# Kernel tuning notes

Hardware: AMD Instinct MI355X
Metric: run time of the kernel (lower is better)

Reference implementation:

```python
import jax, jax.numpy as jnp
import numpy as np

EPS = 1e-6


def rms_norm(x, w):
    xf = x.astype(jnp.float32)
    var = jnp.mean(xf * xf, axis=-1, keepdims=True)
    return (xf * jax.lax.rsqrt(var + EPS)).astype(x.dtype) * w


def rope_interleaved(x, cos, sin):
    # x: [B, S, D]; rotate interleaved pairs (even=real, odd=imag)
    B, S, D = x.shape
    xp = x.reshape(B, S, D // 2, 2)
    rot = jnp.stack([-xp[..., 1], xp[..., 0]], axis=-1).reshape(B, S, D)
    return (x.astype(jnp.float32) * cos + rot.astype(jnp.float32) * sin).astype(x.dtype)


def setup_inputs() -> dict:
    key = jax.random.key(0)
    ks = jax.random.split(key, 8)
    B, S, D = 1, 2048, 2048
    H, Dh = 32, 64
    std = 1.0 / np.sqrt(D)

    hidden_states = jax.random.normal(ks[0], (B, S, D), jnp.float32)

    # interleaved RoPE tables tiled across heads -> [1, S, D]
    pos = np.arange(S, dtype=np.float64)
    inv_freq = 1.0 / (10000.0 ** (np.arange(0, Dh, 2, dtype=np.float64) / Dh))
    ang = pos[:, None] * inv_freq[None, :]          # [S, Dh/2]
    ang = np.repeat(ang, 2, axis=-1)                 # [S, Dh] interleaved
    ang = np.tile(ang, (1, H))                       # [S, D]
    cos = jnp.asarray(np.cos(ang)[None], jnp.float32)
    sin = jnp.asarray(np.sin(ang)[None], jnp.float32)

    Wq = jax.random.normal(ks[1], (D, D), jnp.float32) * std
    Wk = jax.random.normal(ks[2], (D, D), jnp.float32) * std
    Wv = jax.random.normal(ks[3], (D, D), jnp.float32) * std
    Wo = jax.random.normal(ks[4], (D, D), jnp.float32) * std
    bq = jax.random.normal(ks[5], (D,), jnp.float32) * 0.02
    bk = jax.random.normal(ks[6], (D,), jnp.float32) * 0.02
    bv = jax.random.normal(ks[7], (D,), jnp.float32) * 0.02
    bo = jnp.zeros((D,), jnp.float32)
    q_norm_w = jnp.ones((D,), jnp.float32)
    k_norm_w = jnp.ones((D,), jnp.float32)
    return {
        "hidden_states": hidden_states, "cos": cos, "sin": sin,
        "Wq": Wq, "bq": bq, "Wk": Wk, "bk": bk, "Wv": Wv, "bv": bv,
        "q_norm_w": q_norm_w, "k_norm_w": k_norm_w, "Wo": Wo, "bo": bo,
    }


def reference(hidden_states, cos, sin, Wq, bq, Wk, bk, Wv, bv, q_norm_w, k_norm_w, Wo, bo):
    B, S, D = hidden_states.shape
    H, Dh = 32, 64
    # QKV projections (self-attention: encoder_hidden_states = hidden_states)
    q = hidden_states @ Wq + bq
    k = hidden_states @ Wk + bk
    v = hidden_states @ Wv + bv
    # RMSNorm across heads (over full inner_dim)
    q = rms_norm(q, q_norm_w)
    k = rms_norm(k, k_norm_w)
    # interleaved rotary embedding (key uses query rope when key rope is None)
    q = rope_interleaved(q, cos, sin)
    k = rope_interleaved(k, cos, sin)
    # split heads: [B, H, S, Dh]
    q = q.reshape(B, S, H, Dh).transpose(0, 2, 1, 3)
    k = k.reshape(B, S, H, Dh).transpose(0, 2, 1, 3)
    v = v.reshape(B, S, H, Dh).transpose(0, 2, 1, 3)
    # scaled dot-product attention (no mask, not causal)
    scale = 1.0 / jnp.sqrt(jnp.asarray(Dh, q.dtype))
    scores = jnp.einsum("bhqd,bhkd->bhqk", q, k) * scale
    attn = jax.nn.softmax(scores, axis=-1)
    out = jnp.einsum("bhqk,bhkd->bhqd", attn, v)
    out = out.transpose(0, 2, 1, 3).reshape(B, S, H * Dh)
    return out @ Wo + bo
```

## Files before the change

kernel.cpp:

```cpp
#include <hip/hip_runtime.h>
#include <hip/hip_bf16.h>

typedef __bf16 bf16_t;
typedef __bf16 bf16x8 __attribute__((ext_vector_type(8)));
typedef __bf16 bf16x4 __attribute__((ext_vector_type(4)));
typedef float floatx4 __attribute__((ext_vector_type(4)));
typedef float floatx16 __attribute__((ext_vector_type(16)));

#define S_LEN 2048
#define D_DIM 2048
#define NHEADS 32
#define DH 64

__device__ __forceinline__ void gll16(const bf16_t* g, bf16_t* l) {
    __builtin_amdgcn_global_load_lds(
        (const __attribute__((address_space(1))) unsigned int*)g,
        (__attribute__((address_space(3))) unsigned int*)l, 16, 0, 0);
}

#define BAR()    asm volatile("s_barrier" ::: "memory")
#define WAIT(N)  asm volatile("s_waitcnt vmcnt(" #N ")" ::: "memory")
#define DSWAIT() asm volatile("s_waitcnt lgkmcnt(0)" ::: "memory")

__global__ __launch_bounds__(256) void k_prep(
    const float* __restrict__ hs, bf16_t* __restrict__ Xb,
    const float* __restrict__ W0, const float* __restrict__ W1,
    const float* __restrict__ W2, const float* __restrict__ W3,
    bf16_t* __restrict__ T0, bf16_t* __restrict__ T1,
    bf16_t* __restrict__ T2, bf16_t* __restrict__ T3)
{
    const int t = threadIdx.x;
    if (blockIdx.z == 4) {
        const int bid = blockIdx.y * 32 + blockIdx.x;
        const int i = (bid * 256 + t) * 16;
        const float4 a0 = *(const float4*)(hs + i);
        const float4 a1 = *(const float4*)(hs + i + 4);
        const float4 a2 = *(const float4*)(hs + i + 8);
        const float4 a3 = *(const float4*)(hs + i + 12);
        bf16x8 o0, o1;
        o0[0]=(bf16_t)a0.x; o0[1]=(bf16_t)a0.y; o0[2]=(bf16_t)a0.z; o0[3]=(bf16_t)a0.w;
        o0[4]=(bf16_t)a1.x; o0[5]=(bf16_t)a1.y; o0[6]=(bf16_t)a1.z; o0[7]=(bf16_t)a1.w;
        o1[0]=(bf16_t)a2.x; o1[1]=(bf16_t)a2.y; o1[2]=(bf16_t)a2.z; o1[3]=(bf16_t)a2.w;
        o1[4]=(bf16_t)a3.x; o1[5]=(bf16_t)a3.y; o1[6]=(bf16_t)a3.z; o1[7]=(bf16_t)a3.w;
        *(bf16x8*)(Xb + i) = o0;
        *(bf16x8*)(Xb + i + 8) = o1;
        return;
    }
    const float* W; bf16_t* T;
    switch (blockIdx.z) {
        case 0: W = W0; T = T0; break;
        case 1: W = W1; T = T1; break;
        case 2: W = W2; T = T2; break;
        default: W = W3; T = T3; break;
    }
    __shared__ float tile_t[64][68];
    const int n0 = blockIdx.x * 64, k0 = blockIdx.y * 64;
    #pragma unroll
    for (int i = 0; i < 16; ++i) {
        const int r = i * 4 + (t >> 6);
        const int c = t & 63;
        tile_t[c][r] = W[(size_t)(k0 + r) * D_DIM + n0 + c];
    }
    __syncthreads();
    #pragma unroll
    for (int j = 0; j < 4; ++j) {
        const int n  = j * 16 + (t >> 4);
        const int k4 = (t & 15) * 4;
        const float4 v = *(const float4*)&tile_t[n][k4];
        bf16x4 pk;
        pk[0] = (bf16_t)v.x; pk[1] = (bf16_t)v.y; pk[2] = (bf16_t)v.z; pk[3] = (bf16_t)v.w;
        *(bf16x4*)(T + (size_t)(n0 + n) * D_DIM + k0 + k4) = pk;
    }
}

#define BM 128
#define BN 128
#define BK 32

__global__ __launch_bounds__(256) void k_gemm_qkv(
    const bf16_t* __restrict__ A,
    const bf16_t* __restrict__ Bt0, const bf16_t* __restrict__ Bt1, const bf16_t* __restrict__ Bt2,
    const float* __restrict__ bias0, const float* __restrict__ bias1, const float* __restrict__ bias2,
    bf16_t* __restrict__ Qout, bf16_t* __restrict__ Kout, bf16_t* __restrict__ VtOut,
    int M, int N, int K)
{
    const bf16_t* Bt; const float* bias;
    if (blockIdx.z == 0)      { Bt = Bt0; bias = bias0; }
    else if (blockIdx.z == 1) { Bt = Bt1; bias = bias1; }
    else                      { Bt = Bt2; bias = bias2; }

    __shared__ bf16_t As[3][BM][BK];
    __shared__ bf16_t Bs[3][BN][BK];

    const int t    = threadIdx.x;
    const int lane = t & 63;
    const int wave = t >> 6;
    const int wm = (wave >> 1) * 64;
    const int wn = (wave & 1) * 64;
    const int bm = blockIdx.y * BM;
    const int bn = blockIdx.x * BN;
    const int lm = lane & 15;
    const int lq = lane >> 4;

    const int srow0 = wave * 32 + (lane >> 2);
    const int srow1 = srow0 + 16;
    const int cp    = lane & 3;
    const int gc0 = cp ^ ((srow0 >> 1) & 3);
    const int gc1 = cp ^ ((srow1 >> 1) & 3);

    const bf16_t* Ag0 = A  + (size_t)(bm + srow0) * K + gc0 * 8;
    const bf16_t* Ag1 = A  + (size_t)(bm + srow1) * K + gc1 * 8;
    const bf16_t* Bg0 = Bt + (size_t)(bn + srow0) * K + gc0 * 8;
    const bf16_t* Bg1 = Bt + (size_t)(bn + srow1) * K + gc1 * 8;

    floatx4 acc[4][4];
    #pragma unroll
    for (int i = 0; i < 4; ++i)
        #pragma unroll
        for (int j = 0; j < 4; ++j)
            #pragma unroll
            for (int r = 0; r < 4; ++r) acc[i][j][r] = 0.f;

    const int NIT = K / BK;
    auto stage = [&](int buf, int k0) {
        gll16(Ag0 + k0, &As[buf][wave * 32][0]);
        gll16(Ag1 + k0, &As[buf][wave * 32 + 16][0]);
        gll16(Bg0 + k0, &Bs[buf][wave * 32][0]);
        gll16(Bg1 + k0, &Bs[buf][wave * 32 + 16][0]);
    };
    stage(0, 0);
    stage(1, BK);

    for (int i = 0; i < NIT; ++i) {
        BAR();
        if (i + 2 < NIT) {
            stage((i + 2) % 3, (i + 2) * BK);
            WAIT(8);
        } else if (i + 1 < NIT) {
            WAIT(4);
        } else {
            WAIT(0);
        }
        BAR();

        const int buf = i % 3;
        bf16x8 af[4], bfr[4];
        #pragma unroll
        for (int ii = 0; ii < 4; ++ii) {
            const int row = wm + ii * 16 + lm;
            af[ii] = *(const bf16x8*)&As[buf][row][(lq ^ ((row >> 1) & 3)) * 8];
        }
        #pragma unroll
        for (int j = 0; j < 4; ++j) {
            const int row = wn + j * 16 + lm;
            bfr[j] = *(const bf16x8*)&Bs[buf][row][(lq ^ ((row >> 1) & 3)) * 8];
        }
        #pragma unroll
        for (int ii = 0; ii < 4; ++ii)
            #pragma unroll
            for (int j = 0; j < 4; ++j)
                acc[ii][j] = __builtin_amdgcn_mfma_f32_16x16x32_bf16(af[ii], bfr[j], acc[ii][j], 0, 0, 0);
    }

    if (blockIdx.z == 2) {
        #pragma unroll
        for (int i = 0; i < 4; ++i) {
            const int row0 = bm + wm + i * 16 + lq * 4;
            #pragma unroll
            for (int j = 0; j < 4; ++j) {
                const int col = bn + wn + j * 16 + lm;
                const float bb = bias[col];
                bf16x4 pk;
                #pragma unroll
                for (int r = 0; r < 4; ++r) pk[r] = (bf16_t)(acc[i][j][r] + bb);
                *(bf16x4*)(VtOut + (size_t)col * M + row0) = pk;
            }
        }
    } else {
        bf16_t* C = (blockIdx.z == 0) ? Qout : Kout;
        #pragma unroll
        for (int i = 0; i < 4; ++i) {
            const int row0 = bm + wm + i * 16 + lq * 4;
            #pragma unroll
            for (int j = 0; j < 4; ++j) {
                const int col = bn + wn + j * 16 + lm;
                const float bb = bias[col];
                #pragma unroll
                for (int r = 0; r < 4; ++r)
                    C[(size_t)(row0 + r) * N + col] = (bf16_t)(acc[i][j][r] + bb);
            }
        }
    }
}

__global__ __launch_bounds__(256) void k_gemm_splitk(
    const bf16_t* __restrict__ A, const bf16_t* __restrict__ Bt,
    float* __restrict__ P0, float* __restrict__ P1, float* __restrict__ P2,
    int M, int N, int K)
{
    __shared__ bf16_t As[3][BM][BK];
    __shared__ bf16_t Bs[3][BN][BK];

    const int t    = threadIdx.x;
    const int lane = t & 63;
    const int wave = t >> 6;
    const int wm = (wave >> 1) * 64;
    const int wn = (wave & 1) * 64;
    const int bm = blockIdx.y * BM;
    const int bn = blockIdx.x * BN;
    const int lm = lane & 15;
    const int lq = lane >> 4;
    const int z  = blockIdx.z;

    const int nit_all = K / BK;
    const int it0 = (z * nit_all) / 3;
    const int it1 = ((z + 1) * nit_all) / 3;
    const int NIT = it1 - it0;
    const int kbase = it0 * BK;

    const int srow0 = wave * 32 + (lane >> 2);
    const int srow1 = srow0 + 16;
    const int cp    = lane & 3;
    const int gc0 = cp ^ ((srow0 >> 1) & 3);
    const int gc1 = cp ^ ((srow1 >> 1) & 3);

    const bf16_t* Ag0 = A  + (size_t)(bm + srow0) * K + kbase + gc0 * 8;
    const bf16_t* Ag1 = A  + (size_t)(bm + srow1) * K + kbase + gc1 * 8;
    const bf16_t* Bg0 = Bt + (size_t)(bn + srow0) * K + kbase + gc0 * 8;
    const bf16_t* Bg1 = Bt + (size_t)(bn + srow1) * K + kbase + gc1 * 8;

    floatx4 acc[4][4];
    #pragma unroll
    for (int i = 0; i < 4; ++i)
        #pragma unroll
        for (int j = 0; j < 4; ++j)
            #pragma unroll
            for (int r = 0; r < 4; ++r) acc[i][j][r] = 0.f;

    auto stage = [&](int buf, int k0) {
        gll16(Ag0 + k0, &As[buf][wave * 32][0]);
        gll16(Ag1 + k0, &As[buf][wave * 32 + 16][0]);
        gll16(Bg0 + k0, &Bs[buf][wave * 32][0]);
        gll16(Bg1 + k0, &Bs[buf][wave * 32 + 16][0]);
    };
    stage(0, 0);
    if (1 < NIT) stage(1, BK);

    for (int i = 0; i < NIT; ++i) {
        BAR();
        if (i + 2 < NIT) {
            stage((i + 2) % 3, (i + 2) * BK);
            WAIT(8);
        } else if (i + 1 < NIT) {
            WAIT(4);
        } else {
            WAIT(0);
        }
        BAR();

        const int buf = i % 3;
        bf16x8 af[4], bfr[4];
        #pragma unroll
        for (int ii = 0; ii < 4; ++ii) {
            const int row = wm + ii * 16 + lm;
            af[ii] = *(const bf16x8*)&As[buf][row][(lq ^ ((row >> 1) & 3)) * 8];
        }
        #pragma unroll
        for (int j = 0; j < 4; ++j) {
            const int row = wn + j * 16 + lm;
            bfr[j] = *(const bf16x8*)&Bs[buf][row][(lq ^ ((row >> 1) & 3)) * 8];
        }
        #pragma unroll
        for (int ii = 0; ii < 4; ++ii)
            #pragma unroll
            for (int j = 0; j < 4; ++j)
                acc[ii][j] = __builtin_amdgcn_mfma_f32_16x16x32_bf16(af[ii], bfr[j], acc[ii][j], 0, 0, 0);
    }

    float* C = (z == 0) ? P0 : (z == 1) ? P1 : P2;
    #pragma unroll
    for (int i = 0; i < 4; ++i) {
        const int row0 = bm + wm + i * 16 + lq * 4;
        #pragma unroll
        for (int j = 0; j < 4; ++j) {
            const int col = bn + wn + j * 16 + lm;
            #pragma unroll
            for (int r = 0; r < 4; ++r)
                C[(size_t)(row0 + r) * N + col] = acc[i][j][r];
        }
    }
}

__global__ __launch_bounds__(256) void k_reduce_bias(
    const float* __restrict__ P0, const float* __restrict__ P1,
    const float* __restrict__ P2, const float* __restrict__ bias,
    float* __restrict__ out)
{
    const int i = (blockIdx.x * 256 + threadIdx.x) * 4;
    const float4 b  = *(const float4*)(bias + (i & (D_DIM - 1)));
    const float4 a0 = *(const float4*)(P0 + i);
    const float4 a1 = *(const float4*)(P1 + i);
    const float4 a2 = *(const float4*)(P2 + i);
    float4 o;
    o.x = b.x + a0.x + a1.x + a2.x;
    o.y = b.y + a0.y + a1.y + a2.y;
    o.z = b.z + a0.z + a1.z + a2.z;
    o.w = b.w + a0.w + a1.w + a2.w;
    *(float4*)(out + i) = o;
}

__global__ __launch_bounds__(256) void k_norm_rope(
    bf16_t* __restrict__ Q, bf16_t* __restrict__ Kb_,
    const float* __restrict__ qw, const float* __restrict__ kw,
    const float* __restrict__ cosb, const float* __restrict__ sinb)
{
    bf16_t* X = (blockIdx.z == 0) ? Q : Kb_;
    const float* w = (blockIdx.z == 0) ? qw : kw;
    const int row = blockIdx.x;
    const int t = threadIdx.x;
    const size_t base = (size_t)row * D_DIM + t * 8;

    const bf16x8 xv = *(const bf16x8*)(X + base);
    float x[8];
    #pragma unroll
    for (int i = 0; i < 8; ++i) x[i] = (float)xv[i];

    float ss = 0.f;
    #pragma unroll
    for (int i = 0; i < 8; ++i) ss += x[i] * x[i];
    #pragma unroll
    for (int off = 32; off; off >>= 1) ss += __shfl_xor(ss, off);
    __shared__ float red[4];
    if ((t & 63) == 0) red[t >> 6] = ss;
    __syncthreads();
    const float tot = red[0] + red[1] + red[2] + red[3];
    const float rms = rsqrtf(tot * (1.0f / D_DIM) + 1e-6f);

    float wv[8], c[8], sn[8];
    { float4 a = *(const float4*)(w + t * 8); float4 b = *(const float4*)(w + t * 8 + 4);
      wv[0]=a.x; wv[1]=a.y; wv[2]=a.z; wv[3]=a.w; wv[4]=b.x; wv[5]=b.y; wv[6]=b.z; wv[7]=b.w; }
    const size_t cbase = (size_t)row * D_DIM + ((t * 8) & 63);
    { float4 a = *(const float4*)(cosb + cbase); float4 b = *(const float4*)(cosb + cbase + 4);
      c[0]=a.x; c[1]=a.y; c[2]=a.z; c[3]=a.w; c[4]=b.x; c[5]=b.y; c[6]=b.z; c[7]=b.w; }
    { float4 a = *(const float4*)(sinb + cbase); float4 b = *(const float4*)(sinb + cbase + 4);
      sn[0]=a.x; sn[1]=a.y; sn[2]=a.z; sn[3]=a.w; sn[4]=b.x; sn[5]=b.y; sn[6]=b.z; sn[7]=b.w; }

    bf16x8 o;
    #pragma unroll
    for (int p = 0; p < 4; ++p) {
        const float e  = x[2*p]     * rms * wv[2*p];
        const float od = x[2*p + 1] * rms * wv[2*p + 1];
        o[2*p]     = (bf16_t)(e * c[2*p]     - od * sn[2*p]);
        o[2*p + 1] = (bf16_t)(od * c[2*p + 1] + e * sn[2*p + 1]);
    }
    *(bf16x8*)(X + base) = o;
}

#define LDPQ 72

__global__ __launch_bounds__(256) void k_flash(
    const bf16_t* __restrict__ Qb, const bf16_t* __restrict__ Kb,
    const bf16_t* __restrict__ Vt, bf16_t* __restrict__ Ob)
{
    const int bid = blockIdx.x;
    const int jj  = bid >> 3;
    const int h   = ((bid & 7) << 2) | (jj >> 4);
    const int qblk = jj & 15;
    const int hc = h * DH;
    const int t = threadIdx.x;
    const int wave = t >> 6, lane = t & 63;
    const int ln = lane & 31, hf = lane >> 5;
    const int qw = qblk * 128 + wave * 32;

    __shared__ bf16_t Ks[3][64][64];
    __shared__ bf16_t Vs[3][64][64];
    __shared__ bf16_t Ps[4][32][LDPQ];
    __shared__ float  Lw[4][32];

    bf16x8 bq[4];
    #pragma unroll
    for (int kt = 0; kt < 4; ++kt)
        bq[kt] = *(const bf16x8*)(Qb + (size_t)(qw + ln) * D_DIM + hc + kt * 16 + hf * 8);

    const int r0  = wave * 16 + (lane >> 3);
    const int r1  = r0 + 8;
    const int cp8 = lane & 7;
    const int gcA = cp8 ^ (r0 & 7);
    const int gcB = cp8 ^ (r1 & 7);
    const bf16_t* kg0 = Kb + (size_t)r0 * D_DIM + hc + gcA * 8;
    const bf16_t* kg1 = Kb + (size_t)r1 * D_DIM + hc + gcB * 8;
    const bf16_t* vg0 = Vt + (size_t)(hc + r0) * S_LEN + gcA * 8;
    const bf16_t* vg1 = Vt + (size_t)(hc + r1) * S_LEN + gcB * 8;

    auto stageKV = [&](int buf, int kc) {
        gll16(kg0 + (size_t)kc * D_DIM, &Ks[buf][wave * 16][0]);
        gll16(kg1 + (size_t)kc * D_DIM, &Ks[buf][wave * 16 + 8][0]);
        gll16(vg0 + kc, &Vs[buf][wave * 16][0]);
        gll16(vg1 + kc, &Vs[buf][wave * 16 + 8][0]);
    };

    floatx16 o0, o1;
    #pragma unroll
    for (int r = 0; r < 16; ++r) { o0[r] = 0.f; o1[r] = 0.f; }
    float lsum = 0.f;

    const int swz = ln & 7;
    const float c_exp = 0.125f * 1.44269504089f;
    const int NCH = S_LEN / 64;

    auto qk = [&](int buf, floatx16& s0, floatx16& s1) {
        #pragma unroll
        for (int r = 0; r < 16; ++r) { s0[r] = 0.f; s1[r] = 0.f; }
        #pragma unroll
        for (int kt = 0; kt < 4; ++kt) {
            const int ch = 2 * kt + hf;
            const bf16x8 a0 = *(const bf16x8*)&Ks[buf][ln]     [(ch ^ swz) * 8];
            const bf16x8 a1 = *(const bf16x8*)&Ks[buf][32 + ln][(ch ^ swz) * 8];
            s0 = __builtin_amdgcn_mfma_f32_32x32x16_bf16(a0, bq[kt], s0, 0, 0, 0);
            s1 = __builtin_amdgcn_mfma_f32_32x32x16_bf16(a1, bq[kt], s1, 0, 0, 0);
        }
    };
    auto expv = [&](const floatx16& s0, const floatx16& s1) {
        #pragma unroll
        for (int g = 0; g < 4; ++g) {
            bf16x4 p0, p1;
            #pragma unroll
            for (int r4 = 0; r4 < 4; ++r4) {
                const float e0 = __builtin_amdgcn_exp2f(s0[4 * g + r4] * c_exp);
                const float e1 = __builtin_amdgcn_exp2f(s1[4 * g + r4] * c_exp);
                p0[r4] = (bf16_t)e0; p1[r4] = (bf16_t)e1;
                lsum += e0 + e1;
            }
            *(bf16x4*)&Ps[wave][ln][8 * g + 4 * hf]      = p0;
            *(bf16x4*)&Ps[wave][ln][32 + 8 * g + 4 * hf] = p1;
        }
    };
    auto pv = [&](int buf) {
        #pragma unroll
        for (int kt = 0; kt < 4; ++kt) {
            const int ch = 2 * kt + hf;
            const bf16x8 ap  = *(const bf16x8*)&Ps[wave][ln][kt * 16 + hf * 8];
            const bf16x8 bv0 = *(const bf16x8*)&Vs[buf][ln]     [(ch ^ swz) * 8];
            const bf16x8 bv1 = *(const bf16x8*)&Vs[buf][32 + ln][(ch ^ swz) * 8];
            o0 = __builtin_amdgcn_mfma_f32_32x32x16_bf16(ap, bv0, o0, 0, 0, 0);
            o1 = __builtin_amdgcn_mfma_f32_32x32x16_bf16(ap, bv1, o1, 0, 0, 0);
        }
    };

    stageKV(0, 0);
    stageKV(1, 64);

    floatx16 stA0, stA1, stB0, stB1;

    auto pipe_step = [&](int c, floatx16& n0_, floatx16& n1_,
                         floatx16& p0_, floatx16& p1_) {
        BAR();
        if (c >= 1 && c + 1 < NCH) {
            stageKV((c + 1) % 3, (c + 1) * 64);
            WAIT(4);
        } else if (c == 0) {
            WAIT(4);
        } else {
            WAIT(0);
        }
        BAR();
        qk(c % 3, n0_, n1_);
        if (c > 0) {
            expv(p0_, p1_);
            DSWAIT();
            pv((c - 1) % 3);
        }
    };

    for (int c2 = 0; c2 < NCH; c2 += 2) {
        pipe_step(c2,     stA0, stA1, stB0, stB1);
        pipe_step(c2 + 1, stB0, stB1, stA0, stA1);
    }
    expv(stB0, stB1);
    DSWAIT();
    pv((NCH - 1) % 3);

    const float ltot = lsum + __shfl_xor(lsum, 32);
    if (hf == 0) Lw[wave][ln] = ltot;
    DSWAIT();
    float4 li[4];
    li[0] = *(const float4*)&Lw[wave][4 * hf];
    li[1] = *(const float4*)&Lw[wave][8 + 4 * hf];
    li[2] = *(const float4*)&Lw[wave][16 + 4 * hf];
    li[3] = *(const float4*)&Lw[wave][24 + 4 * hf];

    #pragma unroll
    for (int r = 0; r < 16; ++r) {
        const int row = (r & 3) + 8 * (r >> 2) + 4 * hf;
        const float lv = (r & 3) == 0 ? li[r >> 2].x : (r & 3) == 1 ? li[r >> 2].y
                       : (r & 3) == 2 ? li[r >> 2].z : li[r >> 2].w;
        const float inv = 1.0f / lv;
        Ob[(size_t)(qw + row) * D_DIM + hc + ln]      = (bf16_t)(o0[r] * inv);
        Ob[(size_t)(qw + row) * D_DIM + hc + 32 + ln] = (bf16_t)(o1[r] * inv);
    }
}

extern "C" void kernel_launch(void* const* d_in, const int* in_sizes, int n_in,
                              void* d_out, int out_size, void* d_ws, size_t ws_size,
                              hipStream_t stream) {
    const float* hs   = (const float*)d_in[0];
    const float* cosb = (const float*)d_in[1];
    const float* sinb = (const float*)d_in[2];
    const float* Wq   = (const float*)d_in[3];
    const float* bq   = (const float*)d_in[4];
    const float* Wk   = (const float*)d_in[5];
    const float* bk   = (const float*)d_in[6];
    const float* Wv   = (const float*)d_in[7];
    const float* bv   = (const float*)d_in[8];
    const float* qw   = (const float*)d_in[9];
    const float* kw   = (const float*)d_in[10];
    const float* Wo   = (const float*)d_in[11];
    const float* bo   = (const float*)d_in[12];
    float* out = (float*)d_out;

    char* ws = (char*)d_ws;
    bf16_t* Xb  = (bf16_t*)(ws);
    bf16_t* Wqt = (bf16_t*)(ws + ((size_t)8  << 20));
    bf16_t* Wkt = (bf16_t*)(ws + ((size_t)16 << 20));
    bf16_t* Wvt = (bf16_t*)(ws + ((size_t)24 << 20));
    bf16_t* Wot = (bf16_t*)(ws + ((size_t)32 << 20));
    bf16_t* Qb  = (bf16_t*)(ws + ((size_t)40 << 20));
    bf16_t* Kb  = (bf16_t*)(ws + ((size_t)48 << 20));
    bf16_t* Vt  = (bf16_t*)(ws + ((size_t)56 << 20));
    bf16_t* Ob  = (bf16_t*)(ws + ((size_t)64 << 20));
    float*  P0  = (float*) (ws);
    float*  P1  = (float*) (ws + ((size_t)16 << 20));
    float*  P2  = (float*) (ws + ((size_t)48 << 20));

    const int n = S_LEN * D_DIM;

    k_prep<<<dim3(32, 32, 5), 256, 0, stream>>>(hs, Xb, Wq, Wk, Wv, Wo, Wqt, Wkt, Wvt, Wot);

    k_gemm_qkv<<<dim3(D_DIM / BN, S_LEN / BM, 3), 256, 0, stream>>>(
        Xb, Wqt, Wkt, Wvt, bq, bk, bv, Qb, Kb, Vt, S_LEN, D_DIM, D_DIM);

    k_norm_rope<<<dim3(S_LEN, 1, 2), 256, 0, stream>>>(Qb, Kb, qw, kw, cosb, sinb);

    k_flash<<<512, 256, 0, stream>>>(Qb, Kb, Vt, Ob);

    k_gemm_splitk<<<dim3(D_DIM / BN, S_LEN / BM, 3), 256, 0, stream>>>(
        Ob, Wot, P0, P1, P2, S_LEN, D_DIM, D_DIM);
    k_reduce_bias<<<n / (256 * 4), 256, 0, stream>>>(P0, P1, P2, bo, out);
}
```

Baseline: 314.0 us.

## Restructure flash kernel to 2-wave blocks with double buffering and register-held V

The attention kernel now uses 128-thread blocks (two waves, 64 query rows) launched as 1024 blocks, switching from triple to double-buffered K/V staging. V fragments are loaded into registers for the current chunk and consumed one iteration later, so the V LDS buffer can be overwritten earlier. The P tile gets an XOR swizzle instead of padding, and the row-sum scratch reuses the P buffer. The aim is higher occupancy and less LDS per block, at the cost of more blocks each reloading K/V and extra register pressure from the held V fragments.

```diff
diff --git a/kernel.cpp b/kernel.cpp
--- a/kernel.cpp
+++ b/kernel.cpp
@@ -356,138 +356,151 @@
     *(bf16x8*)(X + base) = o;
 }
 
-#define LDPQ 72
-
-__global__ __launch_bounds__(256) void k_flash(
+__global__ __launch_bounds__(128, 2) void k_flash(
     const bf16_t* __restrict__ Qb, const bf16_t* __restrict__ Kb,
     const bf16_t* __restrict__ Vt, bf16_t* __restrict__ Ob)
 {
     const int bid = blockIdx.x;
-    const int jj  = bid >> 3;
-    const int h   = ((bid & 7) << 2) | (jj >> 4);
-    const int qblk = jj & 15;
+    const int h    = ((bid & 7) << 2) | (bid >> 8);
+    const int qblk = (bid >> 3) & 31;
     const int hc = h * DH;
     const int t = threadIdx.x;
     const int wave = t >> 6, lane = t & 63;
     const int ln = lane & 31, hf = lane >> 5;
-    const int qw = qblk * 128 + wave * 32;
-
-    __shared__ bf16_t Ks[3][64][64];
-    __shared__ bf16_t Vs[3][64][64];
-    __shared__ bf16_t Ps[4][32][LDPQ];
-    __shared__ float  Lw[4][32];
+    const int qw = qblk * 64 + wave * 32;
+
+    __shared__ bf16_t Ks[2][64][64];
+    __shared__ bf16_t Vs[2][64][64];
+    __shared__ bf16_t Ps[2][32][64];
 
     bf16x8 bq[4];
     #pragma unroll
     for (int kt = 0; kt < 4; ++kt)
         bq[kt] = *(const bf16x8*)(Qb + (size_t)(qw + ln) * D_DIM + hc + kt * 16 + hf * 8);
 
-    const int r0  = wave * 16 + (lane >> 3);
-    const int r1  = r0 + 8;
-    const int cp8 = lane & 7;
-    const int gcA = cp8 ^ (r0 & 7);
-    const int gcB = cp8 ^ (r1 & 7);
-    const bf16_t* kg0 = Kb + (size_t)r0 * D_DIM + hc + gcA * 8;
-    const bf16_t* kg1 = Kb + (size_t)r1 * D_DIM + hc + gcB * 8;
-    const bf16_t* vg0 = Vt + (size_t)(hc + r0) * S_LEN + gcA * 8;
-    const bf16_t* vg1 = Vt + (size_t)(hc + r1) * S_LEN + gcB * 8;
+    const int rr = wave * 32 + (lane >> 3);
+    const int gc = (lane & 7) ^ (lane >> 3);
+    const bf16_t* kg = Kb + (size_t)rr * D_DIM + hc + gc * 8;
+    const bf16_t* vg = Vt + (size_t)(hc + rr) * S_LEN + gc * 8;
 
     auto stageKV = [&](int buf, int kc) {
-        gll16(kg0 + (size_t)kc * D_DIM, &Ks[buf][wave * 16][0]);
-        gll16(kg1 + (size_t)kc * D_DIM, &Ks[buf][wave * 16 + 8][0]);
-        gll16(vg0 + kc, &Vs[buf][wave * 16][0]);
-        gll16(vg1 + kc, &Vs[buf][wave * 16 + 8][0]);
+        #pragma unroll
+        for (int i = 0; i < 4; ++i) {
+            gll16(kg + (size_t)(kc + 8 * i) * D_DIM, &Ks[buf][wave * 32 + 8 * i][0]);
+            gll16(vg + (size_t)(8 * i) * S_LEN + kc, &Vs[buf][wave * 32 + 8 * i][0]);
+        }
     };
 
-    floatx16 o0, o1;
+    floatx16 o0, o1, st;
     #pragma unroll
     for (int r = 0; r < 16; ++r) { o0[r] = 0.f; o1[r] = 0.f; }
     float lsum = 0.f;
+    bf16x8 vr[2][8];
 
     const int swz = ln & 7;
     const float c_exp = 0.125f * 1.44269504089f;
     const int NCH = S_LEN / 64;
 
-    auto qk = [&](int buf, floatx16& s0, floatx16& s1) {
-        #pragma unroll
-        for (int r = 0; r < 16; ++r) { s0[r] = 0.f; s1[r] = 0.f; }
+    auto qk = [&]() {
+        #pragma unroll
+        for (int r = 0; r < 16; ++r) st[r] = 0.f;
+    };
+    (void)qk;
+
+    floatx16 st1;
+
+    stageKV(0, 0);
+
+    for (int c = 0; c < NCH; ++c) {
+        const int cur = c & 1;
+        BAR();
+        if (c + 1 < NCH) {
+            stageKV(cur ^ 1, (c + 1) * 64);
+            WAIT(8);
+        } else {
+            WAIT(0);
+        }
+        BAR();
+
+        if (c > 0) {
+            #pragma unroll
+            for (int g = 0; g < 4; ++g) {
+                bf16x4 p0, p1;
+                #pragma unroll
+                for (int r4 = 0; r4 < 4; ++r4) {
+                    const float e0 = __builtin_amdgcn_exp2f(st[4 * g + r4] * c_exp);
+                    const float e1 = __builtin_amdgcn_exp2f(st1[4 * g + r4] * c_exp);
+                    p0[r4] = (bf16_t)e0; p1[r4] = (bf16_t)e1;
+                    lsum += e0 + e1;
+                }
+                *(bf16x4*)&Ps[wave][ln][((0 + g) ^ swz) * 8 + 4 * hf] = p0;
+                *(bf16x4*)&Ps[wave][ln][((4 + g) ^ swz) * 8 + 4 * hf] = p1;
+            }
+        }
+
+        #pragma unroll
+        for (int r = 0; r < 16; ++r) { st[r] = 0.f; st1[r] = 0.f; }
         #pragma unroll
         for (int kt = 0; kt < 4; ++kt) {
             const int ch = 2 * kt + hf;
-            const bf16x8 a0 = *(const bf16x8*)&Ks[buf][ln]     [(ch ^ swz) * 8];
-            const bf16x8 a1 = *(const bf16x8*)&Ks[buf][32 + ln][(ch ^ swz) * 8];
-            s0 = __builtin_amdgcn_mfma_f32_32x32x16_bf16(a0, bq[kt], s0, 0, 0, 0);
-            s1 = __builtin_amdgcn_mfma_f32_32x32x16_bf16(a1, bq[kt], s1, 0, 0, 0);
-        }
-    };
-    auto expv = [&](const floatx16& s0, const floatx16& s1) {
-        #pragma unroll
-        for (int g = 0; g < 4; ++g) {
-            bf16x4 p0, p1;
-            #pragma unroll
-            for (int r4 = 0; r4 < 4; ++r4) {
-                const float e0 = __builtin_amdgcn_exp2f(s0[4 * g + r4] * c_exp);
-                const float e1 = __builtin_amdgcn_exp2f(s1[4 * g + r4] * c_exp);
-                p0[r4] = (bf16_t)e0; p1[r4] = (bf16_t)e1;
-                lsum += e0 + e1;
-            }
-            *(bf16x4*)&Ps[wave][ln][8 * g + 4 * hf]      = p0;
-            *(bf16x4*)&Ps[wave][ln][32 + 8 * g + 4 * hf] = p1;
-        }
-    };
-    auto pv = [&](int buf) {
+            const bf16x8 a0 = *(const bf16x8*)&Ks[cur][ln]     [(ch ^ swz) * 8];
+            const bf16x8 a1 = *(const bf16x8*)&Ks[cur][32 + ln][(ch ^ swz) * 8];
+            st  = __builtin_amdgcn_mfma_f32_32x32x16_bf16(a0, bq[kt], st,  0, 0, 0);
+            st1 = __builtin_amdgcn_mfma_f32_32x32x16_bf16(a1, bq[kt], st1, 0, 0, 0);
+        }
+
         #pragma unroll
         for (int kt = 0; kt < 4; ++kt) {
             const int ch = 2 * kt + hf;
-            const bf16x8 ap  = *(const bf16x8*)&Ps[wave][ln][kt * 16 + hf * 8];
-            const bf16x8 bv0 = *(const bf16x8*)&Vs[buf][ln]     [(ch ^ swz) * 8];
-            const bf16x8 bv1 = *(const bf16x8*)&Vs[buf][32 + ln][(ch ^ swz) * 8];
-            o0 = __builtin_amdgcn_mfma_f32_32x32x16_bf16(ap, bv0, o0, 0, 0, 0);
-            o1 = __builtin_amdgcn_mfma_f32_32x32x16_bf16(ap, bv1, o1, 0, 0, 0);
-        }
-    };
-
-    stageKV(0, 0);
-    stageKV(1, 64);
-
-    floatx16 stA0, stA1, stB0, stB1;
-
-    auto pipe_step = [&](int c, floatx16& n0_, floatx16& n1_,
-                         floatx16& p0_, floatx16& p1_) {
-        BAR();
-        if (c >= 1 && c + 1 < NCH) {
-            stageKV((c + 1) % 3, (c + 1) * 64);
-            WAIT(4);
-        } else if (c == 0) {
-            WAIT(4);
-        } else {
-            WAIT(0);
-        }
-        BAR();
-        qk(c % 3, n0_, n1_);
+            vr[cur][kt]     = *(const bf16x8*)&Vs[cur][ln]     [(ch ^ swz) * 8];
+            vr[cur][4 + kt] = *(const bf16x8*)&Vs[cur][32 + ln][(ch ^ swz) * 8];
+        }
+
         if (c > 0) {
-            expv(p0_, p1_);
             DSWAIT();
-            pv((c - 1) % 3);
-        }
-    };
-
-    for (int c2 = 0; c2 < NCH; c2 += 2) {
-        pipe_step(c2,     stA0, stA1, stB0, stB1);
-        pipe_step(c2 + 1, stB0, stB1, stA0, stA1);
-    }
-    expv(stB0, stB1);
+            #pragma unroll
+            for (int kt = 0; kt < 4; ++kt) {
+                const bf16x8 ap = *(const bf16x8*)&Ps[wave][ln][((2 * kt + hf) ^ swz) * 8];
+                o0 = __builtin_amdgcn_mfma_f32_32x32x16_bf16(ap, vr[cur ^ 1][kt],     o0, 0, 0, 0);
+                o1 = __builtin_amdgcn_mfma_f32_32x32x16_bf16(ap, vr[cur ^ 1][4 + kt], o1, 0, 0, 0);
+            }
+        }
+        DSWAIT();
+    }
+
+    #pragma unroll
+    for (int g = 0; g < 4; ++g) {
+        bf16x4 p0, p1;
+        #pragma unroll
+        for (int r4 = 0; r4 < 4; ++r4) {
+            const float e0 = __builtin_amdgcn_exp2f(st[4 * g + r4] * c_exp);
+            const float e1 = __builtin_amdgcn_exp2f(st1[4 * g + r4] * c_exp);
+            p0[r4] = (bf16_t)e0; p1[r4] = (bf16_t)e1;
+            lsum += e0 + e1;
+        }
+        *(bf16x4*)&Ps[wave][ln][((0 + g) ^ swz) * 8 + 4 * hf] = p0;
+        *(bf16x4*)&Ps[wave][ln][((4 + g) ^ swz) * 8 + 4 * hf] = p1;
+    }
     DSWAIT();
-    pv((NCH - 1) % 3);
-
+    {
+        const int last = (NCH - 1) & 1;
+        #pragma unroll
+        for (int kt = 0; kt < 4; ++kt) {
+            const bf16x8 ap = *(const bf16x8*)&Ps[wave][ln][((2 * kt + hf) ^ swz) * 8];
+            o0 = __builtin_amdgcn_mfma_f32_32x32x16_bf16(ap, vr[last][kt],     o0, 0, 0, 0);
+            o1 = __builtin_amdgcn_mfma_f32_32x32x16_bf16(ap, vr[last][4 + kt], o1, 0, 0, 0);
+        }
+    }
+
+    float* Lwp = (float*)&Ps[wave][0][0];
     const float ltot = lsum + __shfl_xor(lsum, 32);
-    if (hf == 0) Lw[wave][ln] = ltot;
+    if (hf == 0) Lwp[ln] = ltot;
     DSWAIT();
     float4 li[4];
-    li[0] = *(const float4*)&Lw[wave][4 * hf];
-    li[1] = *(const float4*)&Lw[wave][8 + 4 * hf];
-    li[2] = *(const float4*)&Lw[wave][16 + 4 * hf];
-    li[3] = *(const float4*)&Lw[wave][24 + 4 * hf];
+    li[0] = *(const float4*)&Lwp[4 * hf];
+    li[1] = *(const float4*)&Lwp[8 + 4 * hf];
+    li[2] = *(const float4*)&Lwp[16 + 4 * hf];
+    li[3] = *(const float4*)&Lwp[24 + 4 * hf];
 
     #pragma unroll
     for (int r = 0; r < 16; ++r) {
@@ -541,7 +554,7 @@
 
     k_norm_rope<<<dim3(S_LEN, 1, 2), 256, 0, stream>>>(Qb, Kb, qw, kw, cosb, sinb);
 
-    k_flash<<<512, 256, 0, stream>>>(Qb, Kb, Vt, Ob);
+    k_flash<<<1024, 128, 0, stream>>>(Qb, Kb, Vt, Ob);
 
     k_gemm_splitk<<<dim3(D_DIM / BN, S_LEN / BM, 3), 256, 0, stream>>>(
         Ob, Wot, P0, P1, P2, S_LEN, D_DIM, D_DIM);
```

Result: slower. 404.0 us (+28.7%).
